# Kernel optimization log

Hardware: AMD Instinct MI355X
Metric: run time of the kernel (lower is better)

Reference implementation:

```python
import jax, jax.numpy as jnp
import numpy as np

HIDDEN = 8192
K = 32
DIMS = [512, 768]
BATCH = 16384

def _xavier(key, shape):
    fan_out, fan_in = shape
    limit = np.sqrt(6.0 / (fan_in + fan_out)).astype(np.float32)
    return jax.random.uniform(key, shape, dtype=jnp.float32, minval=-limit, maxval=limit)

def setup_inputs() -> dict:
    key = jax.random.key(0)
    ks = jax.random.split(key, 6)
    return {
        "x0": jax.random.normal(ks[0], (BATCH, DIMS[0]), dtype=jnp.float32),
        "x1": jax.random.normal(ks[1], (BATCH, DIMS[1]), dtype=jnp.float32),
        "pre_bias0": jnp.zeros((DIMS[0],), dtype=jnp.float32),
        "pre_bias1": jnp.zeros((DIMS[1],), dtype=jnp.float32),
        "enc_w0": _xavier(ks[2], (HIDDEN, DIMS[0])),   # nn.Linear(d0, hidden).weight
        "enc_w1": _xavier(ks[3], (HIDDEN, DIMS[1])),
        "dec_w0": _xavier(ks[4], (DIMS[0], HIDDEN)),   # nn.Linear(hidden, d0).weight
        "dec_w1": _xavier(ks[5], (DIMS[1], HIDDEN)),
        "post_bias0": jnp.zeros((DIMS[0],), dtype=jnp.float32),
        "post_bias1": jnp.zeros((DIMS[1],), dtype=jnp.float32),
        "source_idx": 0,
    }

def _topk_sparse(z, k):
    # keep top-k per row, zero the rest (hard TopK activation)
    vals, idx = jax.lax.top_k(z, k)                      # [B, k]
    rows = jnp.arange(z.shape[0])[:, None]               # [B, 1]
    return jnp.zeros_like(z).at[rows, idx].set(vals)

def reference(x0, x1, pre_bias0, pre_bias1, enc_w0, enc_w1,
              dec_w0, dec_w1, post_bias0, post_bias1, source_idx):
    xs = (x0, x1)
    pbs = (pre_bias0, pre_bias1)
    ews = (enc_w0, enc_w1)
    # encode from source model: pre-bias subtract -> linear -> TopK sparsify
    x = xs[source_idx]
    z_dense = (x - pbs[source_idx]) @ ews[source_idx].T   # [B, HIDDEN]
    z = _topk_sparse(z_dense, K)
    # decode to every model's activation space
    rec0 = z @ dec_w0.T + post_bias0                      # [B, d0]
    rec1 = z @ dec_w1.T + post_bias1                      # [B, d1]
    return (z, rec0, rec1)
```

## Files before the change

kernel.cpp:

```cpp
#include <hip/hip_runtime.h>


#define BATCH  16384
#define HIDDEN 8192
#define DIM0   512
#define DIM1   768
#define TOPK   32
#define CAND_MAX 256
#define WIN_LO 36
#define WIN_HI 64

#define KLO_G 0xBECDu
#define KHI_G 0xC020u

typedef __attribute__((ext_vector_type(8))) short bf16x8;
typedef __attribute__((ext_vector_type(8))) unsigned short u16x8;
typedef __attribute__((ext_vector_type(4))) float f32x4;

__device__ __forceinline__ unsigned fkey(float f) {
    unsigned u = __float_as_uint(f);
    return (u & 0x80000000u) ? ~u : (u | 0x80000000u);
}
__device__ __forceinline__ unsigned fkey16(unsigned short h) {
    return (h & 0x8000u) ? (unsigned)((~h) & 0xFFFFu) : (unsigned)(h | 0x8000u);
}
__device__ __forceinline__ unsigned short f2b(float f) {
    unsigned u = __float_as_uint(f);
    unsigned r = (u + 0x7FFFu + ((u >> 16) & 1u)) >> 16;
    return (unsigned short)r;
}
__device__ __forceinline__ float b2f(unsigned short h) {
    return __uint_as_float(((unsigned)h) << 16);
}
__device__ __forceinline__ void load_lds16(const void* g, void* l) {
    __builtin_amdgcn_global_load_lds((const __attribute__((address_space(1))) void*)g,
                                     (__attribute__((address_space(3))) void*)l, 16, 0, 0);
}

template<int SRC>
__device__ __forceinline__ void convert_impl(
    const float* __restrict__ x, const float* __restrict__ pb,
    const float* __restrict__ w,
    unsigned short* __restrict__ xb, unsigned short* __restrict__ wb)
{
    constexpr int D = SRC ? DIM1 : DIM0;
    const int nx4 = BATCH * D / 4;
    const int nw4 = HIDDEN * D / 4;
    for (int i = blockIdx.x * blockDim.x + threadIdx.x; i < nx4 + nw4;
         i += gridDim.x * blockDim.x) {
        if (i < nx4) {
            float4 v = ((const float4*)x)[i];
            const int k = (i * 4) % D;
            v.x -= pb[k]; v.y -= pb[k + 1]; v.z -= pb[k + 2]; v.w -= pb[k + 3];
            ushort4 o; o.x = f2b(v.x); o.y = f2b(v.y); o.z = f2b(v.z); o.w = f2b(v.w);
            ((ushort4*)xb)[i] = o;
        } else {
            const float4 v = ((const float4*)w)[i - nx4];
            ushort4 o; o.x = f2b(v.x); o.y = f2b(v.y); o.z = f2b(v.z); o.w = f2b(v.w);
            ((ushort4*)wb)[i - nx4] = o;
        }
    }
}

__global__ void convert_xw(const float* __restrict__ x0, const float* __restrict__ x1,
                           const float* __restrict__ pb0, const float* __restrict__ pb1,
                           const float* __restrict__ w0, const float* __restrict__ w1,
                           const int* __restrict__ srcp,
                           unsigned short* __restrict__ xb, unsigned short* __restrict__ wb)
{
    if (*srcp == 0) convert_impl<0>(x0, pb0, w0, xb, wb);
    else            convert_impl<1>(x1, pb1, w1, xb, wb);
}

__global__ void transpose_dec_bf16(const float* __restrict__ dec,
                                   unsigned short* __restrict__ decT, int DD)
{
    __shared__ float t[32][33];
    const int hb = blockIdx.x * 32, db = blockIdx.y * 32;
    const int lx = threadIdx.x, ly = threadIdx.y;
#pragma unroll
    for (int s = 0; s < 32; s += 8)
        t[ly + s][lx] = dec[(size_t)(db + ly + s) * HIDDEN + hb + lx];
    __syncthreads();
#pragma unroll
    for (int s = 0; s < 32; s += 8)
        decT[(size_t)(hb + ly + s) * DD + db + lx] = f2b(t[lx][ly + s]);
}

template<int SRC>
__device__ __forceinline__ void gemm_impl(
    const unsigned short* __restrict__ xb, const unsigned short* __restrict__ wb,
    float* __restrict__ z, unsigned short* As, unsigned short* Bs)
{
    constexpr int D = SRC ? DIM1 : DIM0;

    const int nwg = gridDim.x;
    int id = blockIdx.x;
    id = (id & 7) * (nwg >> 3) + (id >> 3);
    const int bx = id & 63;
    const int by = id >> 6;
    const int m0 = by * 128, n0 = bx * 128;

    const int tid  = threadIdx.x;
    const int lane = tid & 63;
    const int wid  = tid >> 6;
    const int wr   = wid >> 1;
    const int wc   = wid & 1;
    const int l15  = lane & 15;
    const int g    = lane >> 4;

    f32x4 acc[4][4];
#pragma unroll
    for (int i = 0; i < 4; ++i)
#pragma unroll
        for (int j = 0; j < 4; ++j) acc[i][j] = (f32x4){0.f, 0.f, 0.f, 0.f};

    for (int k0 = 0; k0 < D; k0 += 64) {
#pragma unroll
        for (int q = 0; q < 4; ++q) {
            const int c   = wid * 256 + q * 64 + lane;
            const int row = c >> 3, jb = c & 7;
            const int j   = jb ^ (row & 7);
            load_lds16(xb + (size_t)(m0 + row) * D + k0 + j * 8,
                       As + (size_t)(wid * 256 + q * 64) * 8);
            load_lds16(wb + (size_t)(n0 + row) * D + k0 + j * 8,
                       Bs + (size_t)(wid * 256 + q * 64) * 8);
        }
        __syncthreads();

#pragma unroll
        for (int kk = 0; kk < 2; ++kk) {
            bf16x8 a[4], b[4];
#pragma unroll
            for (int f = 0; f < 4; ++f) {
                const int rA = wr * 64 + f * 16 + l15;
                const int sA = ((kk * 4 + g) ^ (rA & 7)) * 16;
                a[f] = *(const bf16x8*)((const char*)As + rA * 128 + sA);
                const int rB = wc * 64 + f * 16 + l15;
                const int sB = ((kk * 4 + g) ^ (rB & 7)) * 16;
                b[f] = *(const bf16x8*)((const char*)Bs + rB * 128 + sB);
            }
#pragma unroll
            for (int fi = 0; fi < 4; ++fi)
#pragma unroll
                for (int fj = 0; fj < 4; ++fj)
                    acc[fi][fj] = __builtin_amdgcn_mfma_f32_16x16x32_bf16(
                        a[fi], b[fj], acc[fi][fj], 0, 0, 0);
        }
        __syncthreads();
    }

#pragma unroll
    for (int fi = 0; fi < 4; ++fi) {
        const int row = m0 + wr * 64 + fi * 16 + g * 4;
#pragma unroll
        for (int fj = 0; fj < 4; ++fj) {
            const int col = n0 + wc * 64 + fj * 16 + l15;
#pragma unroll
            for (int r = 0; r < 4; ++r) {
                unsigned short* zs =
                    (unsigned short*)((char*)z + (size_t)(row + r) * (HIDDEN * 4));
                zs[col] = f2b(acc[fi][fj][r]);
            }
        }
    }

    if (bx >= 32) {
        const f32x4 zv = (f32x4){0.f, 0.f, 0.f, 0.f};
        const int c4 = (4096 >> 2) + (bx - 32) * 32 + (tid & 31);
#pragma unroll
        for (int pass = 0; pass < 16; ++pass) {
            const int r = m0 + pass * 8 + (tid >> 5);
            __builtin_nontemporal_store(zv, (f32x4*)(z + (size_t)r * HIDDEN) + c4);
        }
    }
}

__global__ __launch_bounds__(256, 2)
void gemm_bf16(const unsigned short* __restrict__ xb, const unsigned short* __restrict__ wb,
               const int* __restrict__ srcp, float* __restrict__ z)
{
    __shared__ unsigned short As[128 * 64];
    __shared__ unsigned short Bs[128 * 64];
    if (*srcp == 0) gemm_impl<0>(xb, wb, z, As, Bs);
    else            gemm_impl<1>(xb, wb, z, As, Bs);
}

template<int SRC>
__device__ __forceinline__ void topk_impl(
    float* __restrict__ z,
    const float* __restrict__ xsrc, const float* __restrict__ pb,
    const float* __restrict__ ew,
    const unsigned short* __restrict__ dTb0, const unsigned short* __restrict__ dTb1,
    const float* __restrict__ po0, const float* __restrict__ po1,
    float* __restrict__ rec0, float* __restrict__ rec1,
    float* xs, int* cidx, float* cval, unsigned char* cflag,
    int* counts, unsigned* pcounts, int* s_cnt, float* selv, int* seli)
{
    constexpr int D = SRC ? DIM1 : DIM0;

    const int tid = threadIdx.x;
    const size_t row = blockIdx.x;
    float* __restrict__ zrow = z + row * HIDDEN;
    const unsigned short* __restrict__ zsrow =
        (const unsigned short*)((const char*)z + row * (HIDDEN * 4));

    unsigned pkey[16];
#pragma unroll
    for (int s = 0; s < 4; ++s) {
        const u16x8 v = *(const u16x8*)(zsrow + (size_t)(s * 256 + tid) * 8);
#pragma unroll
        for (int p = 0; p < 4; ++p)
            pkey[s * 4 + p] = fkey16(v[2 * p]) | (fkey16(v[2 * p + 1]) << 16);
    }

    const f32x4 zv4 = (f32x4){0.f, 0.f, 0.f, 0.f};
#pragma unroll
    for (int s = 0; s < 4; ++s)
        __builtin_nontemporal_store(zv4, (f32x4*)&zrow[(size_t)(s * 256 + tid) * 4]);

    if (tid < D / 4) {
        const float4 xv = ((const float4*)(xsrc + row * D))[tid];
        const float4 pv = ((const float4*)pb)[tid];
        ((float4*)xs)[tid] = make_float4(xv.x - pv.x, xv.y - pv.y,
                                         xv.z - pv.z, xv.w - pv.w);
    }
    if (tid == 0) *s_cnt = 0;

    {
        int clo = 0, chi = 0;
#pragma unroll
        for (int p = 0; p < 16; ++p) {
            const unsigned klo16 = pkey[p] & 0xFFFFu, khi16 = pkey[p] >> 16;
            clo += (klo16 > KLO_G) ? 1 : 0;  chi += (klo16 > KHI_G) ? 1 : 0;
            clo += (khi16 > KLO_G) ? 1 : 0;  chi += (khi16 > KHI_G) ? 1 : 0;
        }
        unsigned pk = (unsigned)clo | ((unsigned)chi << 16);
#pragma unroll
        for (int off = 32; off; off >>= 1) pk += __shfl_xor(pk, off);
        if ((tid & 63) == 0) pcounts[tid >> 6] = pk;
    }
    __syncthreads();
    const unsigned ptot = pcounts[0] + pcounts[1] + pcounts[2] + pcounts[3];
    const int tot_lo = (int)(ptot & 0xFFFFu), tot_hi = (int)(ptot >> 16);

    unsigned kappa;
    int found = 0;
    if (tot_lo >= WIN_LO && tot_lo <= WIN_HI)      { kappa = KLO_G; found = 1; }
    else if (tot_hi >= WIN_LO && tot_hi <= WIN_HI) { kappa = KHI_G; found = 1; }
    if (!found) {
        unsigned lo = 0u, hi = 65535u;
        if (tot_lo > WIN_HI) lo = KLO_G;
        if (tot_lo < WIN_LO) hi = KLO_G;
        if (tot_hi > WIN_HI) lo = KHI_G;
        if (tot_hi < WIN_LO) hi = (hi < KHI_G) ? hi : KHI_G;
        kappa = lo;
        for (int it = 0; it < 18; ++it) {
            const unsigned mid = (lo + hi) >> 1;
            int c = 0;
#pragma unroll
            for (int p = 0; p < 16; ++p) {
                c += ((pkey[p] & 0xFFFFu) > mid) ? 1 : 0;
                c += ((pkey[p] >> 16)     > mid) ? 1 : 0;
            }
#pragma unroll
            for (int off = 32; off; off >>= 1) c += __shfl_xor(c, off);
            if ((tid & 63) == 0) counts[(it & 1) * 4 + (tid >> 6)] = c;
            __syncthreads();
            const int* cb = counts + (it & 1) * 4;
            const int tot = cb[0] + cb[1] + cb[2] + cb[3];
            if (tot >= WIN_LO && tot <= WIN_HI) { kappa = mid; break; }
            if (tot > WIN_HI) lo = mid; else hi = mid;
            kappa = lo;
            if (hi - lo <= 1u) break;
        }
    }

#pragma unroll
    for (int p = 0; p < 16; ++p) {
#pragma unroll
        for (int h = 0; h < 2; ++h) {
            const unsigned k16 = h ? (pkey[p] >> 16) : (pkey[p] & 0xFFFFu);
            if (k16 > kappa) {
                const int j = 2 * p + h;
                const int slot = atomicAdd(s_cnt, 1);
                if (slot < CAND_MAX)
                    cidx[slot] = ((j >> 3) * 256 + tid) * 8 + (j & 7);
            }
        }
    }
    __syncthreads();
    const int C = min(*s_cnt, CAND_MAX);

    {
        const int grp = tid >> 3, j8 = tid & 7;
        for (int c = grp; c < C; c += 32) {
            const float* __restrict__ wrow = ew + (size_t)cidx[c] * D;
            float4 a4 = make_float4(0.f, 0.f, 0.f, 0.f);
#pragma unroll
            for (int s = 0; s < D; s += 32) {
                const float4 w4 = *(const float4*)&wrow[s + j8 * 4];
                const float4 x4 = *(const float4*)&xs[s + j8 * 4];
                a4.x = fmaf(x4.x, w4.x, a4.x);
                a4.y = fmaf(x4.y, w4.y, a4.y);
                a4.z = fmaf(x4.z, w4.z, a4.z);
                a4.w = fmaf(x4.w, w4.w, a4.w);
            }
            float a = (a4.x + a4.y) + (a4.z + a4.w);
            a += __shfl_xor(a, 1);
            a += __shfl_xor(a, 2);
            a += __shfl_xor(a, 4);
            if (j8 == 0) cval[c] = a;
        }
    }
    __syncthreads();

    if (tid < C) {
        const float v = cval[tid];
        const int  ix = cidx[tid];
        int rank = 0;
        for (int j = 0; j < C; ++j) {
            const float vj = cval[j];
            rank += (vj > v || (vj == v && cidx[j] < ix)) ? 1 : 0;
        }
        cflag[tid] = (rank < TOPK) ? 1 : 0;
    }
    __syncthreads();
    if (tid < C && cflag[tid]) {
        const int ix = cidx[tid];
        int sr = 0;
        for (int j = 0; j < C; ++j) sr += (cflag[j] && cidx[j] < ix) ? 1 : 0;
        selv[sr] = cval[tid];
        seli[sr] = ix;
    }
    __syncthreads();

    if (tid < TOPK) zrow[seli[tid]] = selv[tid];

#pragma unroll
    for (int pass = 0; pass < 2; ++pass) {
        const int slot = pass * 256 + tid;
        if (slot < (DIM0 + DIM1) / 4) {
            const bool is0 = slot < DIM0 / 4;
            const int d0 = is0 ? slot * 4 : (slot - DIM0 / 4) * 4;
            const int DD = is0 ? DIM0 : DIM1;
            const unsigned short* __restrict__ dT = is0 ? dTb0 : dTb1;
            const float* __restrict__ po = is0 ? po0 : po1;
            f32x4 a;
            {
                const float4 p4 = *(const float4*)&po[d0];
                a = (f32x4){p4.x, p4.y, p4.z, p4.w};
            }
#pragma unroll
            for (int j = 0; j < TOPK; ++j) {
                const float sv = selv[j];
                const ushort4 w4 = *(const ushort4*)&dT[(size_t)seli[j] * DD + d0];
                a.x = fmaf(sv, b2f(w4.x), a.x);
                a.y = fmaf(sv, b2f(w4.y), a.y);
                a.z = fmaf(sv, b2f(w4.z), a.z);
                a.w = fmaf(sv, b2f(w4.w), a.w);
            }
            float* __restrict__ out = is0 ? (rec0 + row * DIM0 + d0)
                                          : (rec1 + row * DIM1 + d0);
            __builtin_nontemporal_store(a, (f32x4*)out);
        }
    }
}

__global__ __launch_bounds__(256)
void topk_rescore_decode(float* __restrict__ z,
                         const float* __restrict__ x0, const float* __restrict__ x1,
                         const float* __restrict__ pb0, const float* __restrict__ pb1,
                         const float* __restrict__ ew0, const float* __restrict__ ew1,
                         const unsigned short* __restrict__ dTb0,
                         const unsigned short* __restrict__ dTb1,
                         const float* __restrict__ po0, const float* __restrict__ po1,
                         float* __restrict__ rec0, float* __restrict__ rec1,
                         const int* __restrict__ srcp)
{
    __shared__ float         xs[DIM1];
    __shared__ int           cidx[CAND_MAX];
    __shared__ float         cval[CAND_MAX];
    __shared__ unsigned char cflag[CAND_MAX];
    __shared__ int           counts[2 * 4];
    __shared__ unsigned      pcounts[4];
    __shared__ int           s_cnt;
    __shared__ float         selv[TOPK];
    __shared__ int           seli[TOPK];

    if (*srcp == 0)
        topk_impl<0>(z, x0, pb0, ew0, dTb0, dTb1, po0, po1, rec0, rec1,
                     xs, cidx, cval, cflag, counts, pcounts, &s_cnt, selv, seli);
    else
        topk_impl<1>(z, x1, pb1, ew1, dTb0, dTb1, po0, po1, rec0, rec1,
                     xs, cidx, cval, cflag, counts, pcounts, &s_cnt, selv, seli);
}


__global__ __launch_bounds__(256, 2)
void encode_gemm(const float* __restrict__ x0, const float* __restrict__ x1,
                 const float* __restrict__ pb0, const float* __restrict__ pb1,
                 const float* __restrict__ w0, const float* __restrict__ w1,
                 const int* __restrict__ srcp, float* __restrict__ z)
{
    const int src = *srcp;
    const float* __restrict__ x  = (src == 0) ? x0 : x1;
    const float* __restrict__ pb = (src == 0) ? pb0 : pb1;
    const float* __restrict__ w  = (src == 0) ? w0 : w1;
    const int D = (src == 0) ? DIM0 : DIM1;

    __shared__ float As[16][132];
    __shared__ float Bs[16][132];

    const int tid = threadIdx.x;
    const int m0 = blockIdx.y * 128;
    const int n0 = blockIdx.x * 128;

    const int cA0 = tid,          cA1 = tid + 256;
    const int r0  = cA0 >> 2,     kq0 = (cA0 & 3) * 4;
    const int r1  = cA1 >> 2,     kq1 = (cA1 & 3) * 4;

    const int mf = (tid & 15) * 4;
    const int nf = (tid >> 4) * 4;

    float acc[8][8];
#pragma unroll
    for (int i = 0; i < 8; ++i)
#pragma unroll
        for (int j = 0; j < 8; ++j) acc[i][j] = 0.0f;

    for (int k0 = 0; k0 < D; k0 += 16) {
        const float4 av0 = *(const float4*)(x + (size_t)(m0 + r0) * D + k0 + kq0);
        const float4 av1 = *(const float4*)(x + (size_t)(m0 + r1) * D + k0 + kq1);
        const float4 pv0 = *(const float4*)(pb + k0 + kq0);
        const float4 pv1 = *(const float4*)(pb + k0 + kq1);
        const float4 bv0 = *(const float4*)(w + (size_t)(n0 + r0) * D + k0 + kq0);
        const float4 bv1 = *(const float4*)(w + (size_t)(n0 + r1) * D + k0 + kq1);
        As[kq0 + 0][r0] = av0.x - pv0.x;
        As[kq0 + 1][r0] = av0.y - pv0.y;
        As[kq0 + 2][r0] = av0.z - pv0.z;
        As[kq0 + 3][r0] = av0.w - pv0.w;
        As[kq1 + 0][r1] = av1.x - pv1.x;
        As[kq1 + 1][r1] = av1.y - pv1.y;
        As[kq1 + 2][r1] = av1.z - pv1.z;
        As[kq1 + 3][r1] = av1.w - pv1.w;
        Bs[kq0 + 0][r0] = bv0.x;
        Bs[kq0 + 1][r0] = bv0.y;
        Bs[kq0 + 2][r0] = bv0.z;
        Bs[kq0 + 3][r0] = bv0.w;
        Bs[kq1 + 0][r1] = bv1.x;
        Bs[kq1 + 1][r1] = bv1.y;
        Bs[kq1 + 2][r1] = bv1.z;
        Bs[kq1 + 3][r1] = bv1.w;
        __syncthreads();
#pragma unroll
        for (int kk = 0; kk < 16; ++kk) {
            const float4 A0 = *(const float4*)&As[kk][mf];
            const float4 A1 = *(const float4*)&As[kk][mf + 64];
            const float4 B0 = *(const float4*)&Bs[kk][nf];
            const float4 B1 = *(const float4*)&Bs[kk][nf + 64];
            const float a[8] = {A0.x, A0.y, A0.z, A0.w, A1.x, A1.y, A1.z, A1.w};
            const float b[8] = {B0.x, B0.y, B0.z, B0.w, B1.x, B1.y, B1.z, B1.w};
#pragma unroll
            for (int i = 0; i < 8; ++i)
#pragma unroll
                for (int j = 0; j < 8; ++j)
                    acc[i][j] = fmaf(a[i], b[j], acc[i][j]);
        }
        __syncthreads();
    }

#pragma unroll
    for (int i = 0; i < 8; ++i) {
        const int row = m0 + mf + (i & 3) + (i >> 2) * 64;
        const float4 v0 = make_float4(acc[i][0], acc[i][1], acc[i][2], acc[i][3]);
        const float4 v1 = make_float4(acc[i][4], acc[i][5], acc[i][6], acc[i][7]);
        *(float4*)(z + (size_t)row * HIDDEN + n0 + nf)      = v0;
        *(float4*)(z + (size_t)row * HIDDEN + n0 + nf + 64) = v1;
    }
}

__global__ __launch_bounds__(256, 2)
void topk_decode_fb(float* __restrict__ z,
                    const float* __restrict__ dA, const float* __restrict__ dB,
                    const float* __restrict__ po0, const float* __restrict__ po1,
                    float* __restrict__ rec0, float* __restrict__ rec1)
{
    __shared__ float    rowv[HIDDEN];
    __shared__ unsigned hist[4][257];
    __shared__ unsigned scanbuf[256];
    __shared__ float    selv[TOPK];
    __shared__ int      seli[TOPK];
    __shared__ unsigned sh_byte, sh_gt;

    const int tid = threadIdx.x;
    const size_t rowid = blockIdx.x;
    float* __restrict__ zrow = z + rowid * HIDDEN;

#pragma unroll
    for (int s = 0; s < 8; ++s) {
        const int i4 = s * 256 + tid;
        *(float4*)&rowv[i4 * 4] = *(const float4*)&zrow[i4 * 4];
    }
    __syncthreads();

    unsigned prefix = 0, prefmask = 0, need = TOPK;
#pragma unroll
    for (int p = 3; p >= 0; --p) {
        for (int i = tid; i < 4 * 257; i += 256) (&hist[0][0])[i] = 0;
        __syncthreads();
        const int sh = p * 8;
        for (int s = 0; s < 32; ++s) {
            const int i = s * 256 + tid;
            const unsigned k = fkey(rowv[i]);
            if ((k & prefmask) == prefix)
                atomicAdd(&hist[tid & 3][(k >> sh) & 255], 1);
        }
        __syncthreads();
        const unsigned tot = hist[0][tid] + hist[1][tid] + hist[2][tid] + hist[3][tid];
        hist[0][tid] = tot;
        __syncthreads();
        if (tid == 0) {
            unsigned cum = 0;
            int b = 255;
            for (;; --b) {
                const unsigned c = hist[0][b];
                if (cum + c >= need || b == 0) { sh_byte = (unsigned)b; sh_gt = cum; break; }
                cum += c;
            }
        }
        __syncthreads();
        prefix  |= sh_byte << sh;
        prefmask |= 0xFFu << sh;
        need -= sh_gt;
        __syncthreads();
    }
    const unsigned cut = prefix;
    const unsigned needEq = need;

    unsigned gtmask = 0, eqmask = 0;
#pragma unroll
    for (int j = 0; j < 32; ++j) {
        const int jr = (j + tid) & 31;
        const int i = tid * 32 + jr;
        const unsigned k = fkey(rowv[i]);
        if (k > cut)       gtmask |= 1u << jr;
        else if (k == cut) eqmask |= 1u << jr;
    }

    scanbuf[tid] = __popc(eqmask);
    __syncthreads();
    for (int off = 1; off < 256; off <<= 1) {
        const unsigned v = scanbuf[tid];
        const unsigned add = (tid >= off) ? scanbuf[tid - off] : 0u;
        __syncthreads();
        scanbuf[tid] = v + add;
        __syncthreads();
    }
    const unsigned eqexc = scanbuf[tid] - __popc(eqmask);
    __syncthreads();

    unsigned selmask = gtmask;
    {
        unsigned m = eqmask, r = eqexc;
        while (m) {
            const int j = __ffs(m) - 1;
            if (r < needEq) selmask |= 1u << j;
            ++r;
            m &= m - 1;
        }
    }

    scanbuf[tid] = __popc(selmask);
    __syncthreads();
    for (int off = 1; off < 256; off <<= 1) {
        const unsigned v = scanbuf[tid];
        const unsigned add = (tid >= off) ? scanbuf[tid - off] : 0u;
        __syncthreads();
        scanbuf[tid] = v + add;
        __syncthreads();
    }
    const unsigned selexc = scanbuf[tid] - __popc(selmask);

#pragma unroll
    for (int j = 0; j < 32; ++j) {
        const int jr = (j + tid) & 31;
        const int i = tid * 32 + jr;
        if ((selmask >> jr) & 1u) {
            const int slot = (int)(selexc + __popc(selmask & ((1u << jr) - 1u)));
            selv[slot] = rowv[i];
            seli[slot] = i;
        } else {
            rowv[i] = 0.0f;
        }
    }
    __syncthreads();

#pragma unroll
    for (int s = 0; s < 8; ++s) {
        const int i4 = s * 256 + tid;
        *(float4*)&zrow[i4 * 4] = *(float4*)&rowv[i4 * 4];
    }

    for (int d = tid; d < DIM0; d += 256) {
        float a = po0[d];
#pragma unroll
        for (int j = 0; j < TOPK; ++j)
            a = fmaf(selv[j], dA[(size_t)d * HIDDEN + seli[j]], a);
        rec0[rowid * DIM0 + d] = a;
    }
    for (int d = tid; d < DIM1; d += 256) {
        float a = po1[d];
#pragma unroll
        for (int j = 0; j < TOPK; ++j)
            a = fmaf(selv[j], dB[(size_t)d * HIDDEN + seli[j]], a);
        rec1[rowid * DIM1 + d] = a;
    }
}

extern "C" void kernel_launch(void* const* d_in, const int* in_sizes, int n_in,
                              void* d_out, int out_size, void* d_ws, size_t ws_size,
                              hipStream_t stream)
{
    const float* x0  = (const float*)d_in[0];
    const float* x1  = (const float*)d_in[1];
    const float* pb0 = (const float*)d_in[2];
    const float* pb1 = (const float*)d_in[3];
    const float* ew0 = (const float*)d_in[4];
    const float* ew1 = (const float*)d_in[5];
    const float* dw0 = (const float*)d_in[6];
    const float* dw1 = (const float*)d_in[7];
    const float* po0 = (const float*)d_in[8];
    const float* po1 = (const float*)d_in[9];
    const int*  srcp = (const int*)d_in[10];

    float* z    = (float*)d_out;
    float* rec0 = z + (size_t)BATCH * HIDDEN;
    float* rec1 = rec0 + (size_t)BATCH * DIM0;

    unsigned short* xb   = (unsigned short*)d_ws;
    unsigned short* wb   = xb   + (size_t)BATCH * DIM1;
    unsigned short* dTb0 = wb   + (size_t)HIDDEN * DIM1;
    unsigned short* dTb1 = dTb0 + (size_t)HIDDEN * DIM0;
    const size_t need = ((size_t)BATCH * DIM1 + (size_t)HIDDEN * DIM1 +
                         (size_t)HIDDEN * DIM0 + (size_t)HIDDEN * DIM1) * sizeof(unsigned short);

    if (ws_size >= need) {
        convert_xw<<<4096, 256, 0, stream>>>(x0, x1, pb0, pb1, ew0, ew1, srcp, xb, wb);
        dim3 tb(32, 8);
        transpose_dec_bf16<<<dim3(HIDDEN / 32, DIM0 / 32), tb, 0, stream>>>(dw0, dTb0, DIM0);
        transpose_dec_bf16<<<dim3(HIDDEN / 32, DIM1 / 32), tb, 0, stream>>>(dw1, dTb1, DIM1);
        gemm_bf16<<<(BATCH / 128) * (HIDDEN / 128), 256, 0, stream>>>(xb, wb, srcp, z);
        topk_rescore_decode<<<BATCH, 256, 0, stream>>>(
            z, x0, x1, pb0, pb1, ew0, ew1, dTb0, dTb1, po0, po1, rec0, rec1, srcp);
    } else {
        encode_gemm<<<dim3(HIDDEN / 128, BATCH / 128), 256, 0, stream>>>(
            x0, x1, pb0, pb1, ew0, ew1, srcp, z);
        topk_decode_fb<<<BATCH, 256, 0, stream>>>(z, dw0, dw1, po0, po1, rec0, rec1);
    }
}
```

Baseline: 750.0 us.

## Split top-k screening and rescore/decode into separate kernels via candidate list

Splits the fused per-row top-k kernel in two. The first is a lightweight screening kernel with high occupancy that reads the bf16 keys, zeroes z, and writes a per-row candidate list of up to 128 entries to workspace. The second kernel rescores those candidates in fp32 and runs the decode. The aim is to let the memory-bound screening run at higher occupancy and to shrink the rescore kernel's shared memory and registers, at the cost of an extra launch and a workspace round-trip. The candidate cap also drops from 256 to 128, which risks truncating the list.

```diff
diff --git a/kernel.cpp b/kernel.cpp
--- a/kernel.cpp
+++ b/kernel.cpp
@@ -6,7 +6,7 @@
 #define DIM0   512
 #define DIM1   768
 #define TOPK   32
-#define CAND_MAX 256
+#define LIST_MAX 128
 #define WIN_LO 36
 #define WIN_HI 64
 
@@ -186,18 +186,14 @@
     else            gemm_impl<1>(xb, wb, z, As, Bs);
 }
 
-template<int SRC>
-__device__ __forceinline__ void topk_impl(
-    float* __restrict__ z,
-    const float* __restrict__ xsrc, const float* __restrict__ pb,
-    const float* __restrict__ ew,
-    const unsigned short* __restrict__ dTb0, const unsigned short* __restrict__ dTb1,
-    const float* __restrict__ po0, const float* __restrict__ po1,
-    float* __restrict__ rec0, float* __restrict__ rec1,
-    float* xs, int* cidx, float* cval, unsigned char* cflag,
-    int* counts, unsigned* pcounts, int* s_cnt, float* selv, int* seli)
-{
-    constexpr int D = SRC ? DIM1 : DIM0;
+__global__ __launch_bounds__(256, 8)
+void screen_topk(float* __restrict__ z, int* __restrict__ cnt,
+                 unsigned short* __restrict__ clist)
+{
+    __shared__ int                           counts[2 * 4];
+    __shared__ unsigned                      pcounts[4];
+    __shared__ int                           s_cnt;
+    __shared__ __align__(16) unsigned short  lidx[LIST_MAX];
 
     const int tid = threadIdx.x;
     const size_t row = blockIdx.x;
@@ -219,13 +215,7 @@
     for (int s = 0; s < 4; ++s)
         __builtin_nontemporal_store(zv4, (f32x4*)&zrow[(size_t)(s * 256 + tid) * 4]);
 
-    if (tid < D / 4) {
-        const float4 xv = ((const float4*)(xsrc + row * D))[tid];
-        const float4 pv = ((const float4*)pb)[tid];
-        ((float4*)xs)[tid] = make_float4(xv.x - pv.x, xv.y - pv.y,
-                                         xv.z - pv.z, xv.w - pv.w);
-    }
-    if (tid == 0) *s_cnt = 0;
+    if (tid == 0) s_cnt = 0;
 
     {
         int clo = 0, chi = 0;
@@ -283,21 +273,60 @@
             const unsigned k16 = h ? (pkey[p] >> 16) : (pkey[p] & 0xFFFFu);
             if (k16 > kappa) {
                 const int j = 2 * p + h;
-                const int slot = atomicAdd(s_cnt, 1);
-                if (slot < CAND_MAX)
-                    cidx[slot] = ((j >> 3) * 256 + tid) * 8 + (j & 7);
-            }
-        }
-    }
-    __syncthreads();
-    const int C = min(*s_cnt, CAND_MAX);
+                const int slot = atomicAdd(&s_cnt, 1);
+                if (slot < LIST_MAX)
+                    lidx[slot] = (unsigned short)(((j >> 3) * 256 + tid) * 8 + (j & 7));
+            }
+        }
+    }
+    __syncthreads();
+
+    if (tid == 0) cnt[row] = min(s_cnt, LIST_MAX);
+    if (tid < LIST_MAX / 4)
+        ((ushort4*)(clist + row * LIST_MAX))[tid] = ((const ushort4*)lidx)[tid];
+}
+
+template<int SRC>
+__device__ __forceinline__ void rescore_impl(
+    float* __restrict__ z,
+    const float* __restrict__ xsrc, const float* __restrict__ pb,
+    const float* __restrict__ ew,
+    const unsigned short* __restrict__ dTb0, const unsigned short* __restrict__ dTb1,
+    const float* __restrict__ po0, const float* __restrict__ po1,
+    float* __restrict__ rec0, float* __restrict__ rec1,
+    const int* __restrict__ cnt, const unsigned short* __restrict__ clist,
+    float* xs, int* cidx, float* cval, unsigned char* cflag, float* selv, int* seli)
+{
+    constexpr int D = SRC ? DIM1 : DIM0;
+
+    const int tid = threadIdx.x;
+    const size_t row = blockIdx.x;
+    float* __restrict__ zrow = z + row * HIDDEN;
+
+    const int C = min(cnt[row], LIST_MAX);
+
+    if (tid < LIST_MAX / 4) {
+        const ushort4 w4 = ((const ushort4*)(clist + row * LIST_MAX))[tid];
+        cidx[tid * 4 + 0] = w4.x;
+        cidx[tid * 4 + 1] = w4.y;
+        cidx[tid * 4 + 2] = w4.z;
+        cidx[tid * 4 + 3] = w4.w;
+    }
+
+    if (tid < D / 4) {
+        const float4 xv = ((const float4*)(xsrc + row * D))[tid];
+        const float4 pv = ((const float4*)pb)[tid];
+        ((float4*)xs)[tid] = make_float4(xv.x - pv.x, xv.y - pv.y,
+                                         xv.z - pv.z, xv.w - pv.w);
+    }
+    __syncthreads();
 
     {
         const int grp = tid >> 3, j8 = tid & 7;
         for (int c = grp; c < C; c += 32) {
             const float* __restrict__ wrow = ew + (size_t)cidx[c] * D;
             float4 a4 = make_float4(0.f, 0.f, 0.f, 0.f);
-#pragma unroll
+#pragma unroll 4
             for (int s = 0; s < D; s += 32) {
                 const float4 w4 = *(const float4*)&wrow[s + j8 * 4];
                 const float4 x4 = *(const float4*)&xs[s + j8 * 4];
@@ -368,32 +397,30 @@
 }
 
 __global__ __launch_bounds__(256)
-void topk_rescore_decode(float* __restrict__ z,
-                         const float* __restrict__ x0, const float* __restrict__ x1,
-                         const float* __restrict__ pb0, const float* __restrict__ pb1,
-                         const float* __restrict__ ew0, const float* __restrict__ ew1,
-                         const unsigned short* __restrict__ dTb0,
-                         const unsigned short* __restrict__ dTb1,
-                         const float* __restrict__ po0, const float* __restrict__ po1,
-                         float* __restrict__ rec0, float* __restrict__ rec1,
-                         const int* __restrict__ srcp)
+void rescore_decode(float* __restrict__ z,
+                    const float* __restrict__ x0, const float* __restrict__ x1,
+                    const float* __restrict__ pb0, const float* __restrict__ pb1,
+                    const float* __restrict__ ew0, const float* __restrict__ ew1,
+                    const unsigned short* __restrict__ dTb0,
+                    const unsigned short* __restrict__ dTb1,
+                    const float* __restrict__ po0, const float* __restrict__ po1,
+                    float* __restrict__ rec0, float* __restrict__ rec1,
+                    const int* __restrict__ srcp,
+                    const int* __restrict__ cnt, const unsigned short* __restrict__ clist)
 {
     __shared__ float         xs[DIM1];
-    __shared__ int           cidx[CAND_MAX];
-    __shared__ float         cval[CAND_MAX];
-    __shared__ unsigned char cflag[CAND_MAX];
-    __shared__ int           counts[2 * 4];
-    __shared__ unsigned      pcounts[4];
-    __shared__ int           s_cnt;
+    __shared__ int           cidx[LIST_MAX];
+    __shared__ float         cval[LIST_MAX];
+    __shared__ unsigned char cflag[LIST_MAX];
     __shared__ float         selv[TOPK];
     __shared__ int           seli[TOPK];
 
     if (*srcp == 0)
-        topk_impl<0>(z, x0, pb0, ew0, dTb0, dTb1, po0, po1, rec0, rec1,
-                     xs, cidx, cval, cflag, counts, pcounts, &s_cnt, selv, seli);
+        rescore_impl<0>(z, x0, pb0, ew0, dTb0, dTb1, po0, po1, rec0, rec1,
+                        cnt, clist, xs, cidx, cval, cflag, selv, seli);
     else
-        topk_impl<1>(z, x1, pb1, ew1, dTb0, dTb1, po0, po1, rec0, rec1,
-                     xs, cidx, cval, cflag, counts, pcounts, &s_cnt, selv, seli);
+        rescore_impl<1>(z, x1, pb1, ew1, dTb0, dTb1, po0, po1, rec0, rec1,
+                        cnt, clist, xs, cidx, cval, cflag, selv, seli);
 }
 
 
@@ -642,8 +669,12 @@
     unsigned short* wb   = xb   + (size_t)BATCH * DIM1;
     unsigned short* dTb0 = wb   + (size_t)HIDDEN * DIM1;
     unsigned short* dTb1 = dTb0 + (size_t)HIDDEN * DIM0;
+    int*            cnt  = (int*)(dTb1 + (size_t)HIDDEN * DIM1);
+    unsigned short* clist = (unsigned short*)(cnt + BATCH);
     const size_t need = ((size_t)BATCH * DIM1 + (size_t)HIDDEN * DIM1 +
-                         (size_t)HIDDEN * DIM0 + (size_t)HIDDEN * DIM1) * sizeof(unsigned short);
+                         (size_t)HIDDEN * DIM0 + (size_t)HIDDEN * DIM1) * sizeof(unsigned short)
+                        + (size_t)BATCH * sizeof(int)
+                        + (size_t)BATCH * LIST_MAX * sizeof(unsigned short);
 
     if (ws_size >= need) {
         convert_xw<<<4096, 256, 0, stream>>>(x0, x1, pb0, pb1, ew0, ew1, srcp, xb, wb);
@@ -651,8 +682,10 @@
         transpose_dec_bf16<<<dim3(HIDDEN / 32, DIM0 / 32), tb, 0, stream>>>(dw0, dTb0, DIM0);
         transpose_dec_bf16<<<dim3(HIDDEN / 32, DIM1 / 32), tb, 0, stream>>>(dw1, dTb1, DIM1);
         gemm_bf16<<<(BATCH / 128) * (HIDDEN / 128), 256, 0, stream>>>(xb, wb, srcp, z);
-        topk_rescore_decode<<<BATCH, 256, 0, stream>>>(
-            z, x0, x1, pb0, pb1, ew0, ew1, dTb0, dTb1, po0, po1, rec0, rec1, srcp);
+        screen_topk<<<BATCH, 256, 0, stream>>>(z, cnt, clist);
+        rescore_decode<<<BATCH, 256, 0, stream>>>(
+            z, x0, x1, pb0, pb1, ew0, ew1, dTb0, dTb1, po0, po1, rec0, rec1,
+            srcp, cnt, clist);
     } else {
         encode_gemm<<<dim3(HIDDEN / 128, BATCH / 128), 256, 0, stream>>>(
             x0, x1, pb0, pb1, ew0, ew1, srcp, z);
```

New measurement: 787.3 us. 1.05x slower.
